# Kernel tuning notes

Measured on AMD Instinct MI355X. Metric: run time of the kernel, lower is better.

The kernel has to match this reference:

```python
import jax, jax.numpy as jnp
import numpy as np

T, B, C = 2048, 8, 1024
H, K, P = 16, 31, 15  # num_heads, kernel_size, padding_l
R = C // H


def setup_inputs() -> dict:
    key = jax.random.key(0)
    k1, k2 = jax.random.split(key)
    x = jax.random.normal(k1, (T, B, C), dtype=jnp.float32)
    # weight_linear.weight, xavier-ish scale, shape (H*K, C)
    W = jax.random.normal(k2, (H * K, C), dtype=jnp.float32) * (2.0 / (C + H * K)) ** 0.5
    return {"x": x, "W": W}


def reference(x, W):
    # per-position dynamic kernels: (T,B,H,K)
    w = jnp.einsum('tbc,oc->tbo', x, W).reshape(T, B, H, K)
    w = jax.nn.softmax(w, axis=-1)  # weight_softmax=True
    # depthwise dynamic conv: out[t] = sum_k w[t,:,:,k] * x[t - P + k]
    xr = x.reshape(T, B, H, R)
    xp = jnp.pad(xr, ((P, K - 1 - P), (0, 0), (0, 0), (0, 0)))
    out = jnp.zeros_like(xr)
    for k in range(K):  # fixed small kernel-size loop, fuses under jit
        out = out + w[:, :, :, k:k + 1] * jax.lax.dynamic_slice_in_dim(xp, k, T, axis=0)
    return out.reshape(T, B, C)
```

## Files before the change

kernel.cpp:

```cpp
#include <hip/hip_runtime.h>
#include <cstddef>
#include <cstdint>

constexpr int T_ = 2048;
constexpr int B_ = 8;
constexpr int C_ = 1024;
constexpr int H_ = 16;
constexpr int K_ = 31;
constexpr int P_ = 15;
constexpr int M_ = T_ * B_;
constexpr int N_ = H_ * K_;
constexpr int NP = 512;

typedef _Float16 f16x4 __attribute__((ext_vector_type(4)));
typedef _Float16 f16x8 __attribute__((ext_vector_type(8)));
typedef float f32x4 __attribute__((ext_vector_type(4)));

__device__ __forceinline__ void async_cp16(const void* g, void* l) {
    __builtin_amdgcn_global_load_lds(
        (const __attribute__((address_space(1))) void*)g,
        (__attribute__((address_space(3))) void*)l, 16, 0, 0);
}

constexpr int XCH = M_ * C_ / 8;
constexpr int WCH = NP * C_ / 8;

__global__ __launch_bounds__(256)
void cvt_inputs(const float* __restrict__ X, const float* __restrict__ W,
                _Float16* __restrict__ Xh, _Float16* __restrict__ Wh) {
    const int id = blockIdx.x * 256 + threadIdx.x;
    if (id < XCH) {
        const float4 v0 = *(const float4*)(X + (size_t)id * 8);
        const float4 v1 = *(const float4*)(X + (size_t)id * 8 + 4);
        f16x8 hv;
        hv[0] = (_Float16)v0.x; hv[1] = (_Float16)v0.y;
        hv[2] = (_Float16)v0.z; hv[3] = (_Float16)v0.w;
        hv[4] = (_Float16)v1.x; hv[5] = (_Float16)v1.y;
        hv[6] = (_Float16)v1.z; hv[7] = (_Float16)v1.w;
        *(f16x8*)(Xh + (size_t)id * 8) = hv;
    } else {
        const int j = id - XCH;
        const int n = j >> 7, sp = j & 127;
        const int h = n >> 5, k = n & 31;
        f16x8 hv = {};
        if (k < 31) {
            const float* wp = W + (size_t)(h * 31 + k) * C_ + sp * 8;
            const float4 v0 = *(const float4*)(wp);
            const float4 v1 = *(const float4*)(wp + 4);
            hv[0] = (_Float16)v0.x; hv[1] = (_Float16)v0.y;
            hv[2] = (_Float16)v0.z; hv[3] = (_Float16)v0.w;
            hv[4] = (_Float16)v1.x; hv[5] = (_Float16)v1.y;
            hv[6] = (_Float16)v1.z; hv[7] = (_Float16)v1.w;
        }
        *(f16x8*)(Wh + (size_t)n * C_ + sp * 8) = hv;
    }
}

__global__ __launch_bounds__(256)
void gemm_softmax(const _Float16* __restrict__ Xh,
                  const _Float16* __restrict__ Wh,
                  _Float16* __restrict__ WSM) {
    __shared__ union {
        struct { _Float16 A[3][128 * 64]; _Float16 B[2][128 * 64]; } s;
        _Float16 Ls[128 * 136];
    } u;

    const int tid = threadIdx.x;
    const int lane = tid & 63;
    const int w = tid >> 6;
    const int wm = (w >> 1) * 64;
    const int wn = (w & 1) * 64;
    const int col = lane & 15;
    const int g = lane >> 4;

    const int id = (int)blockIdx.x;
    const int bx = (id & 7) | ((id >> 5) << 3);
    const int by = (id >> 3) & 3;
    const int m0 = bx * 128;
    const int n0 = by * 128;

    const _Float16* asrc[4];
    const _Float16* bsrc[4];
#pragma unroll
    for (int p = 0; p < 4; ++p) {
        const int ci = p * 256 + tid;
        const int r = ci >> 3, cs = ci & 7;
        const int cl = cs ^ (r & 7);
        asrc[p] = Xh + (size_t)(m0 + r) * C_ + cl * 8;
        bsrc[p] = Wh + (size_t)(n0 + r) * C_ + cl * 8;
    }

    f32x4 acc[4][4] = {};

#pragma unroll
    for (int p = 0; p < 4; ++p) {
        const int ci = p * 256 + tid;
        async_cp16(asrc[p], &u.s.A[0][ci * 8]);
    }
#pragma unroll
    for (int p = 0; p < 4; ++p) {
        const int ci = p * 256 + tid;
        async_cp16(bsrc[p], &u.s.B[0][ci * 8]);
    }
#pragma unroll
    for (int p = 0; p < 4; ++p) {
        const int ci = p * 256 + tid;
        async_cp16(asrc[p] + 64, &u.s.A[1][ci * 8]);
    }
    asm volatile("s_waitcnt vmcnt(4)" ::: "memory");
    __builtin_amdgcn_s_barrier();
    __builtin_amdgcn_sched_barrier(0);

    for (int t = 0; t < 16; ++t) {
        const int ca = t % 3, cb = t & 1;
        if (t < 15) {
            const int k1 = (t + 1) * 64;
#pragma unroll
            for (int p = 0; p < 4; ++p) {
                const int ci = p * 256 + tid;
                async_cp16(bsrc[p] + k1, &u.s.B[cb ^ 1][ci * 8]);
            }
        }
        if (t < 14) {
            const int k2 = (t + 2) * 64;
            const int ca2 = (t + 2) % 3;
#pragma unroll
            for (int p = 0; p < 4; ++p) {
                const int ci = p * 256 + tid;
                async_cp16(asrc[p] + k2, &u.s.A[ca2][ci * 8]);
            }
        }

        f16x8 a[2][4], b[2][4];
#pragma unroll
        for (int kk = 0; kk < 2; ++kk) {
#pragma unroll
            for (int mf = 0; mf < 4; ++mf) {
                const int row = wm + mf * 16 + col;
                const int c = ((kk << 2) | g) ^ (row & 7);
                a[kk][mf] = *(const f16x8*)&u.s.A[ca][row * 64 + c * 8];
            }
#pragma unroll
            for (int nf = 0; nf < 4; ++nf) {
                const int row = wn + nf * 16 + col;
                const int c = ((kk << 2) | g) ^ (row & 7);
                b[kk][nf] = *(const f16x8*)&u.s.B[cb][row * 64 + c * 8];
            }
        }
#pragma unroll
        for (int kk = 0; kk < 2; ++kk)
#pragma unroll
            for (int nf = 0; nf < 4; ++nf)
#pragma unroll
                for (int mf = 0; mf < 4; ++mf)
                    acc[mf][nf] = __builtin_amdgcn_mfma_f32_16x16x32_f16(
                        a[kk][mf], b[kk][nf], acc[mf][nf], 0, 0, 0);

        if (t < 14) {
            asm volatile("s_waitcnt vmcnt(4)" ::: "memory");
        } else {
            asm volatile("s_waitcnt vmcnt(0)" ::: "memory");
        }
        __builtin_amdgcn_s_barrier();
        __builtin_amdgcn_sched_barrier(0);
    }

    const int rb = g * 4;
#pragma unroll
    for (int nf = 0; nf < 4; ++nf) {
        const int nl = wn + nf * 16 + col;
#pragma unroll
        for (int mf = 0; mf < 4; ++mf) {
            const int row = wm + mf * 16 + rb;
#pragma unroll
            for (int r = 0; r < 4; ++r)
                u.Ls[(row + r) * 136 + nl] = (_Float16)acc[mf][nf][r];
        }
    }
    __syncthreads();

#pragma unroll
    for (int p = 0; p < 2; ++p) {
        const int task = tid + p * 256;
        const int row = task >> 2, hl = task & 3;
        const _Float16* lp = &u.Ls[row * 136 + hl * 32];
        float v[32];
#pragma unroll
        for (int c = 0; c < 4; ++c) {
            const f16x8 ch = *(const f16x8*)(lp + c * 8);
#pragma unroll
            for (int e = 0; e < 8; ++e) v[c * 8 + e] = (float)ch[e];
        }
        float mx = v[0];
#pragma unroll
        for (int k = 1; k < 31; ++k) mx = fmaxf(mx, v[k]);
        float ssum = 0.f;
#pragma unroll
        for (int k = 0; k < 31; ++k) { v[k] = __expf(v[k] - mx); ssum += v[k]; }
        const float inv = 1.f / ssum;
        _Float16* op = WSM + (size_t)(m0 + row) * NP + n0 + hl * 32;
#pragma unroll
        for (int c = 0; c < 4; ++c) {
            f16x8 ov;
#pragma unroll
            for (int e = 0; e < 8; ++e) {
                const int k = c * 8 + e;
                ov[e] = (k < 31) ? (_Float16)(v[k] * inv) : (_Float16)0.f;
            }
            *(f16x8*)(op + c * 8) = ov;
        }
    }
}

__global__ __launch_bounds__(256)
void dconv(const _Float16* __restrict__ Xh, const _Float16* __restrict__ WSM,
           float* __restrict__ out) {
    __shared__ float xs[94][64];
    __shared__ float ws[64][36];

    const int tid = threadIdx.x;
    const int t0 = blockIdx.x * 64;
    const int bh = (int)blockIdx.y;
    const int b = bh >> 4, h = bh & 15;

    for (int task = tid; task < 94 * 8; task += 256) {
        const int r = task >> 3, hc = task & 7;
        const int tp = t0 + r - 15;
        f16x8 v = {};
        if (tp >= 0 && tp < T_)
            v = *(const f16x8*)(Xh + ((size_t)tp * B_ + b) * C_ + h * 64 + hc * 8);
        f32x4 lo, hi;
        lo[0] = (float)v[0]; lo[1] = (float)v[1];
        lo[2] = (float)v[2]; lo[3] = (float)v[3];
        hi[0] = (float)v[4]; hi[1] = (float)v[5];
        hi[2] = (float)v[6]; hi[3] = (float)v[7];
        const int c0 = (2 * hc) ^ (r & 7), c1 = (2 * hc + 1) ^ (r & 7);
        *(f32x4*)&xs[r][c0 * 4] = lo;
        *(f32x4*)&xs[r][c1 * 4] = hi;
    }
    {
        const int t = tid >> 2, kc = (tid & 3) * 8;
        const f16x8 wv =
            *(const f16x8*)(WSM + ((size_t)(t0 + t) * B_ + b) * NP + h * 32 + kc);
        f32x4 lo, hi;
        lo[0] = (float)wv[0]; lo[1] = (float)wv[1];
        lo[2] = (float)wv[2]; lo[3] = (float)wv[3];
        hi[0] = (float)wv[4]; hi[1] = (float)wv[5];
        hi[2] = (float)wv[6]; hi[3] = (float)wv[7];
        *(f32x4*)&ws[t][kc] = lo;
        *(f32x4*)&ws[t][kc + 4] = hi;
    }
    __syncthreads();

    const int s = tid & 15;
    const int tg4 = (tid >> 4) * 4;
    f32x4 acc[4] = {};
    f32x4 wc[4];

#pragma unroll
    for (int rr = 0; rr < 34; ++rr) {
        const int r = tg4 + rr;
        const f32x4 xv = *(const f32x4*)&xs[r][(s ^ (r & 7)) * 4];
#pragma unroll
        for (int i = 0; i < 4; ++i) {
            const int k = rr - i;
            if (k < 0 || k > 30) continue;
            if ((k & 3) == 0) wc[i] = *(const f32x4*)&ws[tg4 + i][k];
            acc[i] += wc[i][k & 3] * xv;
        }
    }

#pragma unroll
    for (int i = 0; i < 4; ++i) {
        const int t = t0 + tg4 + i;
        *(f32x4*)(out + ((size_t)t * B_ + b) * C_ + h * 64 + s * 4) = acc[i];
    }
}

extern "C" void kernel_launch(void* const* d_in, const int* in_sizes, int n_in,
                              void* d_out, int out_size, void* d_ws,
                              size_t ws_size, hipStream_t stream) {
    const float* X = (const float*)d_in[0];
    const float* W = (const float*)d_in[1];
    float* out = (float*)d_out;

    _Float16* Wh = (_Float16*)d_ws;
    _Float16* WSM = (_Float16*)((char*)d_ws + (size_t)NP * C_ * 2);
    _Float16* Xh = (_Float16*)((char*)d_ws + (size_t)NP * C_ * 2 +
                               (size_t)M_ * NP * 2);

    cvt_inputs<<<(XCH + WCH) / 256, 256, 0, stream>>>(X, W, Xh, Wh);
    gemm_softmax<<<512, 256, 0, stream>>>(Xh, Wh, WSM);
    dconv<<<dim3(T_ / 64, B_ * H_), 256, 0, stream>>>(Xh, WSM, out);
}
```

Baseline: 73.63 us.

## Move softmax from GEMM epilogue into dconv kernel, store raw logits

The GEMM kernel now writes raw fp16 logits straight from accumulators to global memory, dropping the LDS staging and softmax epilogue. The softmax is recomputed inside dconv by 64 threads per block over the weights in fp16 LDS before the convolution. The weight tile in LDS shrinks from fp32 to fp16 and is converted on read. The logit stores are scattered 2-byte global writes instead of vectorized 16-byte ones, and the softmax in dconv runs on only one wave while the other three wait.

```diff
diff --git a/kernel.cpp b/kernel.cpp
--- a/kernel.cpp
+++ b/kernel.cpp
@@ -57,13 +57,11 @@
 }
 
 __global__ __launch_bounds__(256)
-void gemm_softmax(const _Float16* __restrict__ Xh,
-                  const _Float16* __restrict__ Wh,
-                  _Float16* __restrict__ WSM) {
-    __shared__ union {
-        struct { _Float16 A[3][128 * 64]; _Float16 B[2][128 * 64]; } s;
-        _Float16 Ls[128 * 136];
-    } u;
+void gemm_logits(const _Float16* __restrict__ Xh,
+                 const _Float16* __restrict__ Wh,
+                 _Float16* __restrict__ Lg) {
+    __shared__ _Float16 As[3][128 * 64];
+    __shared__ _Float16 Bs[2][128 * 64];
 
     const int tid = threadIdx.x;
     const int lane = tid & 63;
@@ -95,17 +93,17 @@
 #pragma unroll
     for (int p = 0; p < 4; ++p) {
         const int ci = p * 256 + tid;
-        async_cp16(asrc[p], &u.s.A[0][ci * 8]);
-    }
-#pragma unroll
-    for (int p = 0; p < 4; ++p) {
-        const int ci = p * 256 + tid;
-        async_cp16(bsrc[p], &u.s.B[0][ci * 8]);
-    }
-#pragma unroll
-    for (int p = 0; p < 4; ++p) {
-        const int ci = p * 256 + tid;
-        async_cp16(asrc[p] + 64, &u.s.A[1][ci * 8]);
+        async_cp16(asrc[p], &As[0][ci * 8]);
+    }
+#pragma unroll
+    for (int p = 0; p < 4; ++p) {
+        const int ci = p * 256 + tid;
+        async_cp16(bsrc[p], &Bs[0][ci * 8]);
+    }
+#pragma unroll
+    for (int p = 0; p < 4; ++p) {
+        const int ci = p * 256 + tid;
+        async_cp16(asrc[p] + 64, &As[1][ci * 8]);
     }
     asm volatile("s_waitcnt vmcnt(4)" ::: "memory");
     __builtin_amdgcn_s_barrier();
@@ -118,7 +116,7 @@
 #pragma unroll
             for (int p = 0; p < 4; ++p) {
                 const int ci = p * 256 + tid;
-                async_cp16(bsrc[p] + k1, &u.s.B[cb ^ 1][ci * 8]);
+                async_cp16(bsrc[p] + k1, &Bs[cb ^ 1][ci * 8]);
             }
         }
         if (t < 14) {
@@ -127,7 +125,7 @@
 #pragma unroll
             for (int p = 0; p < 4; ++p) {
                 const int ci = p * 256 + tid;
-                async_cp16(asrc[p] + k2, &u.s.A[ca2][ci * 8]);
+                async_cp16(asrc[p] + k2, &As[ca2][ci * 8]);
             }
         }
 
@@ -138,13 +136,13 @@
             for (int mf = 0; mf < 4; ++mf) {
                 const int row = wm + mf * 16 + col;
                 const int c = ((kk << 2) | g) ^ (row & 7);
-                a[kk][mf] = *(const f16x8*)&u.s.A[ca][row * 64 + c * 8];
+                a[kk][mf] = *(const f16x8*)&As[ca][row * 64 + c * 8];
             }
 #pragma unroll
             for (int nf = 0; nf < 4; ++nf) {
                 const int row = wn + nf * 16 + col;
                 const int c = ((kk << 2) | g) ^ (row & 7);
-                b[kk][nf] = *(const f16x8*)&u.s.B[cb][row * 64 + c * 8];
+                b[kk][nf] = *(const f16x8*)&Bs[cb][row * 64 + c * 8];
             }
         }
 #pragma unroll
@@ -154,7 +152,7 @@
 #pragma unroll
                 for (int mf = 0; mf < 4; ++mf)
                     acc[mf][nf] = __builtin_amdgcn_mfma_f32_16x16x32_f16(
-                        a[kk][mf], b[kk][nf], acc[mf][nf], 0, 0, 0);
+                        a[kk][mf], b[kk][nf], acc[kk ? mf : mf][nf], 0, 0, 0);
 
         if (t < 14) {
             asm volatile("s_waitcnt vmcnt(4)" ::: "memory");
@@ -174,49 +172,17 @@
             const int row = wm + mf * 16 + rb;
 #pragma unroll
             for (int r = 0; r < 4; ++r)
-                u.Ls[(row + r) * 136 + nl] = (_Float16)acc[mf][nf][r];
-        }
-    }
-    __syncthreads();
-
-#pragma unroll
-    for (int p = 0; p < 2; ++p) {
-        const int task = tid + p * 256;
-        const int row = task >> 2, hl = task & 3;
-        const _Float16* lp = &u.Ls[row * 136 + hl * 32];
-        float v[32];
-#pragma unroll
-        for (int c = 0; c < 4; ++c) {
-            const f16x8 ch = *(const f16x8*)(lp + c * 8);
-#pragma unroll
-            for (int e = 0; e < 8; ++e) v[c * 8 + e] = (float)ch[e];
-        }
-        float mx = v[0];
-#pragma unroll
-        for (int k = 1; k < 31; ++k) mx = fmaxf(mx, v[k]);
-        float ssum = 0.f;
-#pragma unroll
-        for (int k = 0; k < 31; ++k) { v[k] = __expf(v[k] - mx); ssum += v[k]; }
-        const float inv = 1.f / ssum;
-        _Float16* op = WSM + (size_t)(m0 + row) * NP + n0 + hl * 32;
-#pragma unroll
-        for (int c = 0; c < 4; ++c) {
-            f16x8 ov;
-#pragma unroll
-            for (int e = 0; e < 8; ++e) {
-                const int k = c * 8 + e;
-                ov[e] = (k < 31) ? (_Float16)(v[k] * inv) : (_Float16)0.f;
-            }
-            *(f16x8*)(op + c * 8) = ov;
+                Lg[(size_t)(m0 + row + r) * NP + n0 + nl] =
+                    (_Float16)acc[mf][nf][r];
         }
     }
 }
 
 __global__ __launch_bounds__(256)
-void dconv(const _Float16* __restrict__ Xh, const _Float16* __restrict__ WSM,
+void dconv(const _Float16* __restrict__ Xh, const _Float16* __restrict__ Lg,
            float* __restrict__ out) {
     __shared__ float xs[94][64];
-    __shared__ float ws[64][36];
+    __shared__ _Float16 ws16[64][40];
 
     const int tid = threadIdx.x;
     const int t0 = blockIdx.x * 64;
@@ -241,14 +207,25 @@
     {
         const int t = tid >> 2, kc = (tid & 3) * 8;
         const f16x8 wv =
-            *(const f16x8*)(WSM + ((size_t)(t0 + t) * B_ + b) * NP + h * 32 + kc);
-        f32x4 lo, hi;
-        lo[0] = (float)wv[0]; lo[1] = (float)wv[1];
-        lo[2] = (float)wv[2]; lo[3] = (float)wv[3];
-        hi[0] = (float)wv[4]; hi[1] = (float)wv[5];
-        hi[2] = (float)wv[6]; hi[3] = (float)wv[7];
-        *(f32x4*)&ws[t][kc] = lo;
-        *(f32x4*)&ws[t][kc + 4] = hi;
+            *(const f16x8*)(Lg + ((size_t)(t0 + t) * B_ + b) * NP + h * 32 + kc);
+        *(f16x8*)&ws16[t][kc] = wv;
+    }
+    __syncthreads();
+
+    if (tid < 64) {
+        float v[31];
+        float mx = -1e30f;
+#pragma unroll
+        for (int k = 0; k < 31; ++k) {
+            v[k] = (float)ws16[tid][k];
+            mx = fmaxf(mx, v[k]);
+        }
+        float ssum = 0.f;
+#pragma unroll
+        for (int k = 0; k < 31; ++k) { v[k] = __expf(v[k] - mx); ssum += v[k]; }
+        const float inv = 1.f / ssum;
+#pragma unroll
+        for (int k = 0; k < 31; ++k) ws16[tid][k] = (_Float16)(v[k] * inv);
     }
     __syncthreads();
 
@@ -265,7 +242,11 @@
         for (int i = 0; i < 4; ++i) {
             const int k = rr - i;
             if (k < 0 || k > 30) continue;
-            if ((k & 3) == 0) wc[i] = *(const f32x4*)&ws[tg4 + i][k];
+            if ((k & 3) == 0) {
+                const f16x4 wq = *(const f16x4*)&ws16[tg4 + i][k];
+                wc[i][0] = (float)wq[0]; wc[i][1] = (float)wq[1];
+                wc[i][2] = (float)wq[2]; wc[i][3] = (float)wq[3];
+            }
             acc[i] += wc[i][k & 3] * xv;
         }
     }
@@ -285,11 +266,11 @@
     float* out = (float*)d_out;
 
     _Float16* Wh = (_Float16*)d_ws;
-    _Float16* WSM = (_Float16*)((char*)d_ws + (size_t)NP * C_ * 2);
+    _Float16* Lg = (_Float16*)((char*)d_ws + (size_t)NP * C_ * 2);
     _Float16* Xh = (_Float16*)((char*)d_ws + (size_t)NP * C_ * 2 +
                                (size_t)M_ * NP * 2);
 
     cvt_inputs<<<(XCH + WCH) / 256, 256, 0, stream>>>(X, W, Xh, Wh);
-    gemm_softmax<<<512, 256, 0, stream>>>(Xh, Wh, WSM);
-    dconv<<<dim3(T_ / 64, B_ * H_), 256, 0, stream>>>(Xh, WSM, out);
-}
+    gemm_logits<<<512, 256, 0, stream>>>(Xh, Wh, Lg);
+    dconv<<<dim3(T_ / 64, B_ * H_), 256, 0, stream>>>(Xh, Lg, out);
+}
```

New measurement: 70.15 us. 4.7% less time.
